# Kernel optimization log

Hardware: AMD Instinct MI355X
Metric: run time of the kernel (lower is better)

## Reference

```python
import jax, jax.numpy as jnp
import numpy as np

# Dims (match init_kwargs / input_specs)
N, N_REP, K, D = 8, 2048, 16, 3
C_IN, C_LIFT = 64, 64
C_MID = C_IN + C_LIFT   # 128
C_OUT = 128             # groups=C_OUT -> depthwise since C_MID == C_OUT
EPS = 1e-5


def setup_inputs() -> dict:
    key = jax.random.key(0)
    ks = jax.random.split(key, 10)
    w = lambda i, shape, fan_in: (jax.random.uniform(ks[i], shape, dtype=jnp.float32) * 2.0 - 1.0) / np.float32(np.sqrt(fan_in))
    return dict(
        p=jax.random.normal(ks[0], (N, N_REP, D), dtype=jnp.float32),
        P=jax.random.normal(ks[1], (N, N_REP, K, D), dtype=jnp.float32),
        F=jax.random.normal(ks[2], (N, N_REP, K, C_IN), dtype=jnp.float32),
        # BatchNorm over the D spatial channels (training-mode stats)
        bn_gamma=jnp.ones((D,), dtype=jnp.float32),
        bn_beta=jnp.zeros((D,), dtype=jnp.float32),
        # mlp_lift: Dense(D->C_LIFT) + Dense(C_LIFT->C_LIFT), ELU each
        lift_w1=w(3, (D, C_LIFT), D), lift_b1=jnp.zeros((C_LIFT,), dtype=jnp.float32),
        lift_w2=w(4, (C_LIFT, C_LIFT), C_LIFT), lift_b2=jnp.zeros((C_LIFT,), dtype=jnp.float32),
        # mid_conv: 1x1 Conv2d(D -> K) channels-last == Linear on last dim
        mid_w=w(5, (D, K), D), mid_b=jnp.zeros((K,), dtype=jnp.float32),
        # mlp: Dense(K->K) with ELU
        mlp_w=w(6, (K, K), K), mlp_b=jnp.zeros((K,), dtype=jnp.float32),
        # end_conv: Conv2d(C_MID -> C_OUT, kernel (K,1), groups=C_OUT) == depthwise
        # reduction over the neighbor dim; weight per (out_channel, neighbor)
        end_w=w(7, (C_OUT, K), K), end_b=jnp.zeros((C_OUT,), dtype=jnp.float32),
    )


def reference(p, P, F, bn_gamma, bn_beta, lift_w1, lift_b1, lift_w2, lift_b2,
              mid_w, mid_b, mlp_w, mlp_b, end_w, end_b):
    # Center neighborhoods on the representative point
    P_local = P - p[:, :, None, :]                              # (N,R,K,D)
    # Channels-last BatchNorm over D, batch stats over (N,R,K)
    mean = jnp.mean(P_local, axis=(0, 1, 2), keepdims=True)
    var = jnp.var(P_local, axis=(0, 1, 2), keepdims=True)
    P_norm = (P_local - mean) * jax.lax.rsqrt(var + EPS) * bn_gamma + bn_beta
    # Lift spatial coords to C_LIFT features (MLP of Dense+ELU layers)
    F_lift = jax.nn.elu(P_norm @ lift_w1 + lift_b1)
    F_lift = jax.nn.elu(F_lift @ lift_w2 + lift_b2)             # (N,R,K,C_LIFT)
    F_cat = jnp.concatenate([F_lift, F], axis=-1)               # (N,R,K,C_MID)
    # X-transform: 1x1 conv D->K then Dense(K->K)+ELU -> (N,R,K,K)
    X = P_norm @ mid_w + mid_b
    X = jax.nn.elu(X @ mlp_w + mlp_b)
    # Weighted aggregation: small batched matmul over the neighbor dim
    F_X = jnp.einsum('nrkj,nrjc->nrkc', X, F_cat)               # (N,R,K,C_MID)
    # Depthwise end conv: per-channel weighted sum over neighbors
    F_p = jnp.einsum('nrkc,ck->nrc', F_X, end_w) + end_b        # (N,R,C_OUT)
    return F_p
```

## Files before the change

### kernel.cpp

```cpp
#include <hip/hip_runtime.h>
#include <cstddef>

#define N_TOT   8
#define R_TOT   2048
#define NR_TOT  (N_TOT*R_TOT)
#define KK      16
#define CL      64
#define CM      128
#define EPSV    1e-5f
#define CNTF    262144.0f

typedef float    f32x4  __attribute__((ext_vector_type(4)));
typedef short    bf16x8 __attribute__((ext_vector_type(8)));
typedef unsigned u32x2  __attribute__((ext_vector_type(2)));
typedef unsigned u32x4  __attribute__((ext_vector_type(4)));

union FragU { bf16x8 f; unsigned u[4]; };

__device__ __forceinline__ float elu_f(float x){
    return x > 0.f ? x : (__expf(x) - 1.f);
}

#if defined(__has_builtin) && __has_builtin(__builtin_amdgcn_cvt_pk_bf16_f32)
__device__ __forceinline__ unsigned pk_bf16(float a, float b){
    auto v = __builtin_amdgcn_cvt_pk_bf16_f32(a, b);
    unsigned u; __builtin_memcpy(&u, &v, 4);
    return u;
}
#else
__device__ __forceinline__ unsigned pk_bf16(float a, float b){
    unsigned ua = __float_as_uint(a), ub = __float_as_uint(b);
    ua += 0x7fff + ((ua >> 16) & 1);
    ub += 0x7fff + ((ub >> 16) & 1);
    return (ua >> 16) | (ub & 0xffff0000u);
}
#endif
__device__ __forceinline__ float bf_lo(unsigned u){ return __uint_as_float(u << 16); }
__device__ __forceinline__ float bf_hi(unsigned u){ return __uint_as_float(u & 0xffff0000u); }

__device__ __forceinline__ void split4(const float* x, unsigned* o){
    unsigned h01 = pk_bf16(x[0], x[1]);
    unsigned h23 = pk_bf16(x[2], x[3]);
    float l0 = x[0] - bf_lo(h01), l1 = x[1] - bf_hi(h01);
    float l2 = x[2] - bf_lo(h23), l3 = x[3] - bf_hi(h23);
    o[0] = h01; o[1] = h23; o[2] = pk_bf16(l0, l1); o[3] = pk_bf16(l2, l3);
}

__global__ __launch_bounds__(256) void xconv_stats(
    const float* __restrict__ p, const float* __restrict__ P, float* __restrict__ ws)
{
    const int g = blockIdx.x*256 + threadIdx.x;
    const float4* P4 = (const float4*)(P + (size_t)g*12);
    float4 a = P4[0], b = P4[1], c = P4[2];
    const int nr = g >> 2;
    float pp0 = p[nr*3], pp1 = p[nr*3+1], pp2 = p[nr*3+2];
    float vx0=a.x-pp0, vx1=a.w-pp0, vx2=b.z-pp0, vx3=c.y-pp0;
    float vy0=a.y-pp1, vy1=b.x-pp1, vy2=b.w-pp1, vy3=c.z-pp1;
    float vz0=a.z-pp2, vz1=b.y-pp2, vz2=c.x-pp2, vz3=c.w-pp2;
    float s1[3], s2[3];
    s1[0]=vx0+vx1+vx2+vx3; s2[0]=vx0*vx0+vx1*vx1+vx2*vx2+vx3*vx3;
    s1[1]=vy0+vy1+vy2+vy3; s2[1]=vy0*vy0+vy1*vy1+vy2*vy2+vy3*vy3;
    s1[2]=vz0+vz1+vz2+vz3; s2[2]=vz0*vz0+vz1*vz1+vz2*vz2+vz3*vz3;

    #pragma unroll
    for (int off = 32; off > 0; off >>= 1){
        #pragma unroll
        for (int d = 0; d < 3; d++){
            s1[d] += __shfl_down(s1[d], off, 64);
            s2[d] += __shfl_down(s2[d], off, 64);
        }
    }
    __shared__ float red[4][6];
    int wave = threadIdx.x >> 6, lane = threadIdx.x & 63;
    if (lane == 0){
        #pragma unroll
        for (int d = 0; d < 3; d++){ red[wave][d] = s1[d]; red[wave][3+d] = s2[d]; }
    }
    __syncthreads();
    if (threadIdx.x < 6){
        float v = red[0][threadIdx.x] + red[1][threadIdx.x]
                + red[2][threadIdx.x] + red[3][threadIdx.x];
        atomicAdd(&ws[threadIdx.x], v);
    }
}

__global__ __launch_bounds__(256) void xconv_main(
    const float* __restrict__ p,   const float* __restrict__ P,
    const float* __restrict__ F,
    const float* __restrict__ gamma,const float* __restrict__ beta,
    const float* __restrict__ w1,  const float* __restrict__ b1,
    const float* __restrict__ w2,  const float* __restrict__ b2,
    const float* __restrict__ midw,const float* __restrict__ midb,
    const float* __restrict__ mlpw,const float* __restrict__ mlpb,
    const float* __restrict__ endw,const float* __restrict__ endb,
    const float* __restrict__ ws,  float* __restrict__ out)
{
    __shared__ float    sEndw[128*20];
    __shared__ unsigned sW1[2*64*20];
    __shared__ unsigned sW2[8*64*4];

    const int tid  = threadIdx.x;
    const int lane = tid & 63;
    const int lo16 = lane & 15;
    const int quad = lane >> 4;
    const int wave = tid >> 6;

    if (wave == 0){
        #pragma unroll
        for (int s = 0; s < 2; s++)
            #pragma unroll
            for (int j = 0; j < 8; j++){
                int q = s*32 + quad*8 + j;
                u32x2 v;
                v.x = pk_bf16(w1[q],       w1[64 + q]);
                v.y = pk_bf16(w1[128 + q], b1[q]);
                *(u32x2*)&sW1[(s*64 + lane)*20 + j*2] = v;
            }
    } else if (wave == 1){
        #pragma unroll
        for (int b = 0; b < 4; b++)
            #pragma unroll
            for (int s = 0; s < 2; s++){
                u32x4 f;
                #pragma unroll
                for (int d = 0; d < 4; d++){
                    int q0 = s*32 + quad*8 + d*2;
                    int idx = q0*64 + b*16 + lo16;
                    f[d] = pk_bf16(w2[idx], w2[idx + 64]);
                }
                *(u32x4*)&sW2[((b*2 + s)*64 + lane)*4] = f;
            }
    } else {
        int c = tid - 128;
        const float4* ep = (const float4*)endw;
        #pragma unroll
        for (int i = 0; i < 4; i++)
            *(float4*)&sEndw[c*20 + i*4] = ep[c*4 + i];
    }

    float sc[3], sh[3];
    #pragma unroll
    for (int d = 0; d < 3; d++){
        float mean = ws[d] / CNTF;
        float var  = ws[3+d] / CNTF - mean*mean;
        float s    = gamma[d] * rsqrtf(var + EPSV);
        sc[d] = s; sh[d] = beta[d] - mean*s;
    }
    FragU mlpA[2];
    {
        float mw[4];
        #pragma unroll
        for (int r = 0; r < 4; r++) mw[r] = mlpw[(quad*4 + r)*16 + lo16];
        unsigned o[4]; split4(mw, o);
        mlpA[0].u[0]=o[0]; mlpA[0].u[1]=o[1]; mlpA[0].u[2]=o[0]; mlpA[0].u[3]=o[1];
        mlpA[1].u[0]=o[2]; mlpA[1].u[1]=o[3]; mlpA[1].u[2]=o[2]; mlpA[1].u[3]=o[3];
    }
    float mlpbr[4];
    #pragma unroll
    for (int r = 0; r < 4; r++) mlpbr[r] = mlpb[quad*4 + r];
    float mw0[4], mw1[4], mw2[4], mbv[4];
    #pragma unroll
    for (int j = 0; j < 4; j++){
        int m2 = quad*4 + j;
        mw0[j] = midw[m2]; mw1[j] = midw[16 + m2]; mw2[j] = midw[32 + m2];
        mbv[j] = midb[m2];
    }
    float b2r[4];
    #pragma unroll
    for (int b = 0; b < 4; b++) b2r[b] = b2[b*16 + lo16];
    const float endb0 = endb[lane], endb1 = endb[64 + lane];

    __syncthreads();

    const int wglobal = blockIdx.x*4 + wave;

    #pragma unroll 1
    for (int it = 0; it < 4; it++){
        const int nr = wglobal*4 + it;

        float fv[4][4];
        #pragma unroll
        for (int bt = 0; bt < 4; bt++)
            #pragma unroll
            for (int r = 0; r < 4; r++)
                fv[bt][r] = F[(size_t)nr*1024 + (quad*4 + r)*64 + bt*16 + lo16];
        const int pb = nr*48 + lo16*3;
        float P0 = P[pb], P1 = P[pb+1], P2 = P[pb+2];
        float pp0 = p[nr*3], pp1 = p[nr*3+1], pp2 = p[nr*3+2];

        const float pn0 = (P0 - pp0)*sc[0] + sh[0];
        const float pn1 = (P1 - pp1)*sc[1] + sh[1];
        const float pn2 = (P2 - pp2)*sc[2] + sh[2];

        FragU hf[2];
        #pragma unroll
        for (int s = 0; s < 2; s++){
            const u32x4* wp = (const u32x4*)&sW1[(s*64 + lane)*20];
            #pragma unroll
            for (int d = 0; d < 4; d++){
                u32x4 w = wp[d];
                float h0 = bf_hi(w.y);
                h0 = fmaf(pn0, bf_lo(w.x), h0);
                h0 = fmaf(pn1, bf_hi(w.x), h0);
                h0 = fmaf(pn2, bf_lo(w.y), h0);
                float h1v = bf_hi(w.w);
                h1v = fmaf(pn0, bf_lo(w.z), h1v);
                h1v = fmaf(pn1, bf_hi(w.z), h1v);
                h1v = fmaf(pn2, bf_lo(w.w), h1v);
                hf[s].u[d] = pk_bf16(elu_f(h0), elu_f(h1v));
            }
        }

        float x0[4];
        #pragma unroll
        for (int j = 0; j < 4; j++)
            x0[j] = fmaf(pn2, mw2[j], fmaf(pn1, mw1[j], fmaf(pn0, mw0[j], mbv[j])));
        FragU x0f; split4(x0, x0f.u);

        f32x4 dx = {0.f,0.f,0.f,0.f};
        dx = __builtin_amdgcn_mfma_f32_16x16x32_bf16(mlpA[0].f, x0f.f, dx, 0,0,0);
        dx = __builtin_amdgcn_mfma_f32_16x16x32_bf16(mlpA[1].f, x0f.f, dx, 0,0,0);
        float xv[4];
        #pragma unroll
        for (int r = 0; r < 4; r++) xv[r] = elu_f(dx[r] + mlpbr[r]);
        FragU xA; split4(xv, xA.u);

        float o0 = 0.f, o1 = 0.f;

        #pragma unroll
        for (int b = 0; b < 4; b++){
            FragU wf0, wf1;
            *(u32x4*)wf0.u = *(const u32x4*)&sW2[((b*2 + 0)*64 + lane)*4];
            *(u32x4*)wf1.u = *(const u32x4*)&sW2[((b*2 + 1)*64 + lane)*4];
            f32x4 dl = {0.f,0.f,0.f,0.f};
            dl = __builtin_amdgcn_mfma_f32_16x16x32_bf16(hf[0].f, wf0.f, dl, 0,0,0);
            dl = __builtin_amdgcn_mfma_f32_16x16x32_bf16(hf[1].f, wf1.f, dl, 0,0,0);
            float fl[4];
            #pragma unroll
            for (int r = 0; r < 4; r++) fl[r] = elu_f(dl[r] + b2r[b]);
            FragU bfg;
            unsigned h01 = pk_bf16(fl[0], fl[1]), h23 = pk_bf16(fl[2], fl[3]);
            bfg.u[0] = h01; bfg.u[1] = h23; bfg.u[2] = h01; bfg.u[3] = h23;
            f32x4 da = {0.f,0.f,0.f,0.f};
            da = __builtin_amdgcn_mfma_f32_16x16x32_bf16(xA.f, bfg.f, da, 0,0,0);
            const float4 ew = *(const float4*)&sEndw[(b*16 + lo16)*20 + quad*4];
            float pt = da[0]*ew.x + da[1]*ew.y + da[2]*ew.z + da[3]*ew.w;
            pt += __shfl_xor(pt, 16, 64);
            pt += __shfl_xor(pt, 32, 64);
            if (b == quad) o0 = pt;
        }
        #pragma unroll
        for (int bt = 0; bt < 4; bt++){
            FragU bfg;
            unsigned h01 = pk_bf16(fv[bt][0], fv[bt][1]);
            unsigned h23 = pk_bf16(fv[bt][2], fv[bt][3]);
            bfg.u[0] = h01; bfg.u[1] = h23; bfg.u[2] = h01; bfg.u[3] = h23;
            f32x4 da = {0.f,0.f,0.f,0.f};
            da = __builtin_amdgcn_mfma_f32_16x16x32_bf16(xA.f, bfg.f, da, 0,0,0);
            const float4 ew = *(const float4*)&sEndw[(64 + bt*16 + lo16)*20 + quad*4];
            float pt = da[0]*ew.x + da[1]*ew.y + da[2]*ew.z + da[3]*ew.w;
            pt += __shfl_xor(pt, 16, 64);
            pt += __shfl_xor(pt, 32, 64);
            if (bt == quad) o1 = pt;
        }

        out[(size_t)nr*CM + lane]      = o0 + endb0;
        out[(size_t)nr*CM + 64 + lane] = o1 + endb1;
    }
}

extern "C" void kernel_launch(void* const* d_in, const int* in_sizes, int n_in,
                              void* d_out, int out_size, void* d_ws, size_t ws_size,
                              hipStream_t stream)
{
    const float* p     = (const float*)d_in[0];
    const float* P     = (const float*)d_in[1];
    const float* F     = (const float*)d_in[2];
    const float* gamma = (const float*)d_in[3];
    const float* beta  = (const float*)d_in[4];
    const float* w1    = (const float*)d_in[5];
    const float* b1    = (const float*)d_in[6];
    const float* w2    = (const float*)d_in[7];
    const float* b2    = (const float*)d_in[8];
    const float* midw  = (const float*)d_in[9];
    const float* midb  = (const float*)d_in[10];
    const float* mlpw  = (const float*)d_in[11];
    const float* mlpb  = (const float*)d_in[12];
    const float* endw  = (const float*)d_in[13];
    const float* endb  = (const float*)d_in[14];
    float* ws  = (float*)d_ws;
    float* out = (float*)d_out;

    hipMemsetAsync(d_ws, 0, 32, stream);
    xconv_stats<<<256, 256, 0, stream>>>(p, P, ws);
    xconv_main <<<1024, 256, 0, stream>>>(p, P, F, gamma, beta, w1, b1, w2, b2,
                                          midw, midb, mlpw, mlpb, endw, endb, ws, out);
}
```

Before: 146.8 us.

## Move small weights to LDS, shrink per-wave work, double grid size

Reduces register pressure by moving the mlp, mid_conv and bias constants from per-thread registers into shared memory, and compacts the W1 table, which was duplicated per lane, into a small broadcast layout. F values are packed to bf16 right after loading, so they use half the registers. Each wave now handles 2 points instead of 4 and the grid doubles to 2048 blocks, which adds parallelism and occupancy. In exchange there are more LDS reads per iteration and more per-block setup, since each block repeats the weight staging.

```diff
diff --git a/kernel.cpp b/kernel.cpp
--- a/kernel.cpp
+++ b/kernel.cpp
@@ -96,8 +96,11 @@
     const float* __restrict__ ws,  float* __restrict__ out)
 {
     __shared__ float    sEndw[128*20];
-    __shared__ unsigned sW1[2*64*20];
     __shared__ unsigned sW2[8*64*4];
+    __shared__ unsigned sW1[8*20];
+    __shared__ float    sMid[4*20];
+    __shared__ unsigned sMlpA0[64*4];
+    __shared__ unsigned sMlpA1[64*4];
 
     const int tid  = threadIdx.x;
     const int lane = tid & 63;
@@ -106,16 +109,26 @@
     const int wave = tid >> 6;
 
     if (wave == 0){
-        #pragma unroll
-        for (int s = 0; s < 2; s++)
-            #pragma unroll
-            for (int j = 0; j < 8; j++){
-                int q = s*32 + quad*8 + j;
-                u32x2 v;
-                v.x = pk_bf16(w1[q],       w1[64 + q]);
-                v.y = pk_bf16(w1[128 + q], b1[q]);
-                *(u32x2*)&sW1[(s*64 + lane)*20 + j*2] = v;
+        {
+            int s = lane >> 5, q4 = (lane >> 3) & 3, j = lane & 7;
+            int q = s*32 + q4*8 + j;
+            u32x2 v;
+            v.x = pk_bf16(w1[q],       w1[64 + q]);
+            v.y = pk_bf16(w1[128 + q], b1[q]);
+            *(u32x2*)&sW1[(s*4 + q4)*20 + j*2] = v;
+        }
+        #pragma unroll
+        for (int i = 0; i < 2; i++){
+            int idx = lane + i*64;
+            if (idx < 80){
+                int qq = idx / 20, slot = idx % 20;
+                float val;
+                if (slot < 12)      val = midw[(slot >> 2)*16 + qq*4 + (slot & 3)];
+                else if (slot < 16) val = midb[qq*4 + (slot - 12)];
+                else                val = mlpb[qq*4 + (slot - 16)];
+                sMid[idx] = val;
             }
+        }
     } else if (wave == 1){
         #pragma unroll
         for (int b = 0; b < 4; b++)
@@ -130,12 +143,25 @@
                 }
                 *(u32x4*)&sW2[((b*2 + s)*64 + lane)*4] = f;
             }
+    } else if (wave == 2){
+        const float4* ep = (const float4*)endw;
+        #pragma unroll
+        for (int i = 0; i < 4; i++)
+            *(float4*)&sEndw[lane*20 + i*4] = ep[lane*4 + i];
+        float mw[4];
+        #pragma unroll
+        for (int r = 0; r < 4; r++) mw[r] = mlpw[(quad*4 + r)*16 + lo16];
+        unsigned o[4]; split4(mw, o);
+        u32x4 a0, a1;
+        a0.x=o[0]; a0.y=o[1]; a0.z=o[0]; a0.w=o[1];
+        a1.x=o[2]; a1.y=o[3]; a1.z=o[2]; a1.w=o[3];
+        *(u32x4*)&sMlpA0[lane*4] = a0;
+        *(u32x4*)&sMlpA1[lane*4] = a1;
     } else {
-        int c = tid - 128;
         const float4* ep = (const float4*)endw;
         #pragma unroll
         for (int i = 0; i < 4; i++)
-            *(float4*)&sEndw[c*20 + i*4] = ep[c*4 + i];
+            *(float4*)&sEndw[(64 + lane)*20 + i*4] = ep[(64 + lane)*4 + i];
     }
 
     float sc[3], sh[3];
@@ -146,25 +172,6 @@
         float s    = gamma[d] * rsqrtf(var + EPSV);
         sc[d] = s; sh[d] = beta[d] - mean*s;
     }
-    FragU mlpA[2];
-    {
-        float mw[4];
-        #pragma unroll
-        for (int r = 0; r < 4; r++) mw[r] = mlpw[(quad*4 + r)*16 + lo16];
-        unsigned o[4]; split4(mw, o);
-        mlpA[0].u[0]=o[0]; mlpA[0].u[1]=o[1]; mlpA[0].u[2]=o[0]; mlpA[0].u[3]=o[1];
-        mlpA[1].u[0]=o[2]; mlpA[1].u[1]=o[3]; mlpA[1].u[2]=o[2]; mlpA[1].u[3]=o[3];
-    }
-    float mlpbr[4];
-    #pragma unroll
-    for (int r = 0; r < 4; r++) mlpbr[r] = mlpb[quad*4 + r];
-    float mw0[4], mw1[4], mw2[4], mbv[4];
-    #pragma unroll
-    for (int j = 0; j < 4; j++){
-        int m2 = quad*4 + j;
-        mw0[j] = midw[m2]; mw1[j] = midw[16 + m2]; mw2[j] = midw[32 + m2];
-        mbv[j] = midb[m2];
-    }
     float b2r[4];
     #pragma unroll
     for (int b = 0; b < 4; b++) b2r[b] = b2[b*16 + lo16];
@@ -175,15 +182,23 @@
     const int wglobal = blockIdx.x*4 + wave;
 
     #pragma unroll 1
-    for (int it = 0; it < 4; it++){
-        const int nr = wglobal*4 + it;
-
-        float fv[4][4];
-        #pragma unroll
-        for (int bt = 0; bt < 4; bt++)
-            #pragma unroll
-            for (int r = 0; r < 4; r++)
-                fv[bt][r] = F[(size_t)nr*1024 + (quad*4 + r)*64 + bt*16 + lo16];
+    for (int it = 0; it < 2; it++){
+        const int nr = wglobal*2 + it;
+
+        unsigned fvpk[4][2];
+        {
+            float t[4][4];
+            #pragma unroll
+            for (int bt = 0; bt < 4; bt++)
+                #pragma unroll
+                for (int r = 0; r < 4; r++)
+                    t[bt][r] = F[(size_t)nr*1024 + (quad*4 + r)*64 + bt*16 + lo16];
+            #pragma unroll
+            for (int bt = 0; bt < 4; bt++){
+                fvpk[bt][0] = pk_bf16(t[bt][0], t[bt][1]);
+                fvpk[bt][1] = pk_bf16(t[bt][2], t[bt][3]);
+            }
+        }
         const int pb = nr*48 + lo16*3;
         float P0 = P[pb], P1 = P[pb+1], P2 = P[pb+2];
         float pp0 = p[nr*3], pp1 = p[nr*3+1], pp2 = p[nr*3+2];
@@ -195,7 +210,7 @@
         FragU hf[2];
         #pragma unroll
         for (int s = 0; s < 2; s++){
-            const u32x4* wp = (const u32x4*)&sW1[(s*64 + lane)*20];
+            const u32x4* wp = (const u32x4*)&sW1[(s*4 + quad)*20];
             #pragma unroll
             for (int d = 0; d < 4; d++){
                 u32x4 w = wp[d];
@@ -211,18 +226,22 @@
             }
         }
 
+        const float* md = &sMid[quad*20];
         float x0[4];
         #pragma unroll
         for (int j = 0; j < 4; j++)
-            x0[j] = fmaf(pn2, mw2[j], fmaf(pn1, mw1[j], fmaf(pn0, mw0[j], mbv[j])));
+            x0[j] = fmaf(pn2, md[8+j], fmaf(pn1, md[4+j], fmaf(pn0, md[j], md[12+j])));
         FragU x0f; split4(x0, x0f.u);
 
+        FragU A0, A1;
+        *(u32x4*)A0.u = *(const u32x4*)&sMlpA0[lane*4];
+        *(u32x4*)A1.u = *(const u32x4*)&sMlpA1[lane*4];
         f32x4 dx = {0.f,0.f,0.f,0.f};
-        dx = __builtin_amdgcn_mfma_f32_16x16x32_bf16(mlpA[0].f, x0f.f, dx, 0,0,0);
-        dx = __builtin_amdgcn_mfma_f32_16x16x32_bf16(mlpA[1].f, x0f.f, dx, 0,0,0);
+        dx = __builtin_amdgcn_mfma_f32_16x16x32_bf16(A0.f, x0f.f, dx, 0,0,0);
+        dx = __builtin_amdgcn_mfma_f32_16x16x32_bf16(A1.f, x0f.f, dx, 0,0,0);
         float xv[4];
         #pragma unroll
-        for (int r = 0; r < 4; r++) xv[r] = elu_f(dx[r] + mlpbr[r]);
+        for (int r = 0; r < 4; r++) xv[r] = elu_f(dx[r] + md[16+r]);
         FragU xA; split4(xv, xA.u);
 
         float o0 = 0.f, o1 = 0.f;
@@ -252,9 +271,8 @@
         #pragma unroll
         for (int bt = 0; bt < 4; bt++){
             FragU bfg;
-            unsigned h01 = pk_bf16(fv[bt][0], fv[bt][1]);
-            unsigned h23 = pk_bf16(fv[bt][2], fv[bt][3]);
-            bfg.u[0] = h01; bfg.u[1] = h23; bfg.u[2] = h01; bfg.u[3] = h23;
+            bfg.u[0] = fvpk[bt][0]; bfg.u[1] = fvpk[bt][1];
+            bfg.u[2] = fvpk[bt][0]; bfg.u[3] = fvpk[bt][1];
             f32x4 da = {0.f,0.f,0.f,0.f};
             da = __builtin_amdgcn_mfma_f32_16x16x32_bf16(xA.f, bfg.f, da, 0,0,0);
             const float4 ew = *(const float4*)&sEndw[(64 + bt*16 + lo16)*20 + quad*4];
@@ -293,6 +311,6 @@
 
     hipMemsetAsync(d_ws, 0, 32, stream);
     xconv_stats<<<256, 256, 0, stream>>>(p, P, ws);
-    xconv_main <<<1024, 256, 0, stream>>>(p, P, F, gamma, beta, w1, b1, w2, b2,
+    xconv_main <<<2048, 256, 0, stream>>>(p, P, F, gamma, beta, w1, b1, w2, b2,
                                           midw, midb, mlpw, mlpb, endw, endb, ws, out);
 }
```

Result: slower. 154.9 us (+5.5%).
